# Kernel tuning notes

Hardware: AMD Instinct MI355X
Metric: run time of the kernel (lower is better)

## Reference

```python
import jax, jax.numpy as jnp
import numpy as np

# norse default LIFParameters / LIParameters constants
DT = 1e-3
TAU_SYN_INV = 200.0
TAU_MEM_INV = 100.0
V_LEAK = 0.0
V_TH = 1.0
V_RESET = 0.0
ALPHA = 100.0  # superspike surrogate-gradient slope


@jax.custom_vjp
def superspike(x):
    return (x > 0).astype(x.dtype)

def _ss_fwd(x):
    return (x > 0).astype(x.dtype), x

def _ss_bwd(x, g):
    return (g / (ALPHA * jnp.abs(x) + 1.0) ** 2,)

superspike.defvjp(_ss_fwd, _ss_bwd)


def lif_step(state, inp):
    """norse lif_feed_forward_step: decay v/i, spike on old current, then inject input."""
    v, i = state
    v_dec = v + DT * TAU_MEM_INV * ((V_LEAK - v) + i)
    i_dec = i - DT * TAU_SYN_INV * i
    z = superspike(v_dec - V_TH)
    v_new = (1.0 - z) * v_dec + z * V_RESET
    return z, (v_new, i_dec + inp)


def li_step(state, inp):
    """norse li_feed_forward_step: leaky integrator, output is the membrane voltage."""
    v, i = state
    v_new = v + DT * TAU_MEM_INV * ((V_LEAK - v) + i)
    i_new = i - DT * TAU_SYN_INV * i + inp
    return v_new, (v_new, i_new)


def setup_inputs() -> dict:
    key = jax.random.key(0)
    ks = jax.random.split(key, 5)
    B = 65536
    x = jax.random.normal(ks[0], (B, 1, 10, 10), dtype=jnp.float32)
    conv_w = jax.random.normal(ks[1], (2, 1, 4, 4), dtype=jnp.float32) * 0.3
    conv_b = jax.random.normal(ks[2], (2,), dtype=jnp.float32) * 0.1
    fc_w = jax.random.normal(ks[3], (10, 72), dtype=jnp.float32) * 0.1
    fc_b = jax.random.normal(ks[4], (10,), dtype=jnp.float32) * 0.1
    return {"x": x, "conv_w": conv_w, "conv_b": conv_b, "fc_w": fc_w, "fc_b": fc_b, "num_steps": 64}


def reference(x, conv_w, conv_b, fc_w, fc_b, num_steps):
    B = x.shape[0]
    out_dim = fc_w.shape[0]
    # static input: conv(x) identical at every step, hoist out of the time loop
    g = jax.lax.conv_general_dilated(
        x, conv_w, (1, 1), "VALID",
        dimension_numbers=("NCHW", "OIHW", "NCHW"),
    ) + conv_b[None, :, None, None]  # [B,2,7,7]

    def pool(z):  # MaxPool2d(kernel=2, stride=1), VALID
        return jax.lax.reduce_window(
            z, -jnp.inf, jax.lax.max, (1, 1, 2, 2), (1, 1, 1, 1), "VALID")

    s_lif0 = (jnp.zeros_like(g), jnp.zeros_like(g))                 # [B,2,7,7]
    s_li1_0 = (jnp.zeros((B, 2, 6, 6), x.dtype), jnp.zeros((B, 2, 6, 6), x.dtype))
    s_li2_0 = (jnp.zeros((B, out_dim), x.dtype), jnp.zeros((B, out_dim), x.dtype))

    def step(carry, _):
        s_lif, s1, s2 = carry
        z, s_lif = lif_step(s_lif, g)          # spikes [B,2,7,7]
        z = pool(z)                            # [B,2,6,6]
        z, s1 = li_step(s1, z)                 # LI voltage [B,2,6,6]
        z = z.reshape(B, -1)                   # [B,72]
        z = z @ fc_w.T + fc_b                  # [B,10]
        v, s2 = li_step(s2, z)                 # readout voltage [B,10]
        return (s_lif, s1, s2), None

    (s_lif, s1, s2), _ = jax.lax.scan(step, (s_lif0, s_li1_0, s_li2_0), None, length=num_steps)
    return s2[0]  # final readout membrane voltage [B, output_size]
```

## Files before the change

### kernel.cpp

```cpp
#include <hip/hip_runtime.h>

#define TMAX 64

__global__ __launch_bounds__(256) void snn_fused(
    const float* __restrict__ x,
    const float* __restrict__ conv_w,
    const float* __restrict__ conv_b,
    const float* __restrict__ fc_w,
    const float* __restrict__ fc_b,
    const int*   __restrict__ nsteps,
    float*       __restrict__ out,
    int B)
{
    __shared__ double d_F[TMAX];
    __shared__ float  s_r[TMAX];
    __shared__ float  s_rb[TMAX];
    __shared__ float  s_tab[8][256];
    __shared__ float  s_fcw[720];
    __shared__ float  s_fcb[16];
    __shared__ float  s_cb;

    const int tid = threadIdx.x;
    int T = nsteps[0];
    if (T > TMAX) T = TMAX;
    if (T < 0) T = 0;
    const int tlo = T < 32 ? T : 32;
    const int thi = T > 32 ? (T - 32) : 0;

    if (tid < TMAX) {
        double p9 = 1.0, p8 = 1.0;
        for (int k = 0; k < tid; ++k) { p9 *= 0.9; p8 *= 0.8; }
        d_F[tid] = p9 - p8;
    }
    for (int idx = tid; idx < 720; idx += 256) s_fcw[idx] = fc_w[idx];
    if (tid < 10) s_fcb[tid] = fc_b[tid];
    __syncthreads();

    if (tid < TMAX) {
        double r = 0.0;
        if (tid < T) {
            const int n = T - 1 - tid;
            for (int u = 0; u <= n; ++u) r += d_F[n - u] * d_F[u];
        }
        s_r[tid] = (float)r;
    }
    if (tid == 0) {
        double cb = 0.0;
        for (int m = 0; m < T; ++m) cb += d_F[m];
        s_cb = (float)cb;
    }
    __syncthreads();

    if (tid < 32) {
        s_rb[tid] = (tid < tlo) ? s_r[tlo - 1 - tid] : 0.f;
    } else if (tid < 64) {
        const int p = tid - 32;
        s_rb[tid] = (p < thi) ? s_r[tlo + thi - 1 - p] : 0.f;
    }
    __syncthreads();

    {
        const int v8 = tid;
        #pragma unroll
        for (int k = 0; k < 8; ++k) {
            float ssum = 0.f;
            #pragma unroll
            for (int bb = 0; bb < 8; ++bb)
                if ((v8 >> bb) & 1) ssum += s_rb[k * 8 + bb];
            s_tab[k][v8] = ssum;
        }
    }
    __syncthreads();

    const float cbsum = s_cb;

    const int gt  = blockIdx.x * 256 + tid;
    const int sub = gt & 15;
    const int b   = gt >> 4;
    const int c   = sub >> 3;
    const int y   = sub & 7;
    const int ysim = (y < 6) ? y : 6;
    if (b >= B) return;

    const float* xb = x + b * 100;
    const float cbias = conv_b[c];

    float gg7[7];
    #pragma unroll
    for (int xx = 0; xx < 7; ++xx) gg7[xx] = 0.f;
    {
        float wc[16];
        const float4* wq = reinterpret_cast<const float4*>(conv_w + c * 16);
        #pragma unroll
        for (int k = 0; k < 4; ++k) {
            float4 t = wq[k];
            wc[4*k+0] = t.x; wc[4*k+1] = t.y; wc[4*k+2] = t.z; wc[4*k+3] = t.w;
        }
        #pragma unroll
        for (int ky = 0; ky < 4; ++ky) {
            float xrow[10];
            const float2* q = reinterpret_cast<const float2*>(xb + (ysim + ky) * 10);
            #pragma unroll
            for (int k = 0; k < 5; ++k) { float2 t = q[k]; xrow[2*k] = t.x; xrow[2*k+1] = t.y; }
            #pragma unroll
            for (int xx = 0; xx < 7; ++xx) {
                float a = gg7[xx];
                #pragma unroll
                for (int kx = 0; kx < 4; ++kx)
                    a = __fadd_rn(a, __fmul_rn(wc[ky*4 + kx], xrow[xx + kx]));
                gg7[xx] = a;
            }
        }
    }
    #pragma unroll
    for (int xx = 0; xx < 7; ++xx) gg7[xx] = __fadd_rn(gg7[xx], cbias);

    float v[7], ii[7];
    unsigned int mlo[7], mhi[7];
    float fzero = 0.0f;
    #pragma unroll
    for (int xx = 0; xx < 7; ++xx) { v[xx] = 0.f; ii[xx] = 0.f; mlo[xx] = 0u; mhi[xx] = 0u; }

    #pragma unroll 4
    for (int t = 0; t < tlo; ++t) {
        #pragma unroll
        for (int xx = 0; xx < 7; ++xx) {
            const float imv  = __fsub_rn(ii[xx], v[xx]);
            const float vdec = __fadd_rn(v[xx], __fmul_rn(0.1f, imv));
            const float idec = __fsub_rn(ii[xx], __fmul_rn(0.2f, ii[xx]));
            float vnew;
            asm("v_cmp_lt_f32 vcc, 1.0, %[vd]\n\t"
                "v_cndmask_b32 %[vn], %[vd], %[vz], vcc\n\t"
                "v_addc_co_u32 %[mm], vcc, %[mm], %[mm], vcc"
                : [vn]"=v"(vnew), [mm]"+v"(mlo[xx])
                : [vd]"v"(vdec), [vz]"v"(fzero)
                : "vcc");
            v[xx]  = vnew;
            ii[xx] = __fadd_rn(idec, gg7[xx]);
        }
    }
    #pragma unroll 4
    for (int t = 0; t < thi; ++t) {
        #pragma unroll
        for (int xx = 0; xx < 7; ++xx) {
            const float imv  = __fsub_rn(ii[xx], v[xx]);
            const float vdec = __fadd_rn(v[xx], __fmul_rn(0.1f, imv));
            const float idec = __fsub_rn(ii[xx], __fmul_rn(0.2f, ii[xx]));
            float vnew;
            asm("v_cmp_lt_f32 vcc, 1.0, %[vd]\n\t"
                "v_cndmask_b32 %[vn], %[vd], %[vz], vcc\n\t"
                "v_addc_co_u32 %[mm], vcc, %[mm], %[mm], vcc"
                : [vn]"=v"(vnew), [mm]"+v"(mhi[xx])
                : [vd]"v"(vdec), [vz]"v"(fzero)
                : "vcc");
            v[xx]  = vnew;
            ii[xx] = __fadd_rn(idec, gg7[xx]);
        }
    }

    unsigned int nlo[7], nhi[7];
    #pragma unroll
    for (int xx = 0; xx < 7; ++xx) {
        nlo[xx] = __shfl_down(mlo[xx], 1);
        nhi[xx] = __shfl_down(mhi[xx], 1);
    }

    float outacc[10];
    #pragma unroll
    for (int o = 0; o < 10; ++o) outacc[o] = 0.f;

    if (y < 6) {
        const int jbase = c * 36 + y * 6;
        #pragma unroll
        for (int px = 0; px < 6; ++px) {
            const unsigned int pl = mlo[px] | mlo[px+1] | nlo[px] | nlo[px+1];
            const unsigned int ph = mhi[px] | mhi[px+1] | nhi[px] | nhi[px+1];
            float a = s_tab[0][pl & 255] + s_tab[1][(pl >> 8) & 255]
                    + s_tab[2][(pl >> 16) & 255] + s_tab[3][pl >> 24]
                    + s_tab[4][ph & 255] + s_tab[5][(ph >> 8) & 255]
                    + s_tab[6][(ph >> 16) & 255] + s_tab[7][ph >> 24];
            const int j = jbase + px;
            #pragma unroll
            for (int o = 0; o < 10; ++o)
                outacc[o] = fmaf(s_fcw[o * 72 + j], a, outacc[o]);
        }
    }

    #pragma unroll
    for (int o = 0; o < 10; ++o) {
        float t = outacc[o];
        t += __shfl_xor(t, 1);
        t += __shfl_xor(t, 2);
        t += __shfl_xor(t, 4);
        t += __shfl_xor(t, 8);
        if (sub == 0) out[b * 10 + o] = fmaf(cbsum, s_fcb[o], t);
    }
}

extern "C" void kernel_launch(void* const* d_in, const int* in_sizes, int n_in,
                              void* d_out, int out_size, void* d_ws, size_t ws_size,
                              hipStream_t stream) {
    const float* x      = (const float*)d_in[0];
    const float* conv_w = (const float*)d_in[1];
    const float* conv_b = (const float*)d_in[2];
    const float* fc_w   = (const float*)d_in[3];
    const float* fc_b   = (const float*)d_in[4];
    const int*   nsteps = (const int*)d_in[5];
    float* outp = (float*)d_out;

    const int B = in_sizes[0] / 100;
    const int total = 16 * B;
    const int block = 256;
    const int grid = (total + block - 1) / block;
    snn_fused<<<grid, block, 0, stream>>>(x, conv_w, conv_b, fc_w, fc_b, nsteps, outp, B);
}
```

Measured before the change: 83.30 us.

## Map 14 threads per sample and exchange spike masks via shared memory

Each sample now gets 14 threads (2 channels x 7 rows) instead of 16, so the two padding rows per sample no longer run the 64-step LIF simulation. Blocks grow to 896 threads covering 64 samples. The neighbour-row masks move through LDS instead of wave shuffles, and the per-sample readout reduction becomes an LDS write plus a serial 12-way sum instead of a butterfly shuffle. The extra __syncthreads calls, larger blocks and lower occupancy per CU may offset the cut in simulation work.

Measured after the change: 109.1 us. 30.9% more time.

```diff
diff --git a/kernel.cpp b/kernel.cpp
--- a/kernel.cpp
+++ b/kernel.cpp
@@ -1,8 +1,11 @@
 #include <hip/hip_runtime.h>
 
 #define TMAX 64
-
-__global__ __launch_bounds__(256) void snn_fused(
+#define BPB  64
+#define RPB  14
+#define NTHR (BPB * RPB)
+
+__global__ __launch_bounds__(NTHR) void snn_fused(
     const float* __restrict__ x,
     const float* __restrict__ conv_w,
     const float* __restrict__ conv_b,
@@ -19,6 +22,10 @@
     __shared__ float  s_fcw[720];
     __shared__ float  s_fcb[16];
     __shared__ float  s_cb;
+    __shared__ union {
+        uint2 masks[BPB * RPB * 7];
+        float red[BPB * 12 * 10];
+    } u;
 
     const int tid = threadIdx.x;
     int T = nsteps[0];
@@ -32,7 +39,7 @@
         for (int k = 0; k < tid; ++k) { p9 *= 0.9; p8 *= 0.8; }
         d_F[tid] = p9 - p8;
     }
-    for (int idx = tid; idx < 720; idx += 256) s_fcw[idx] = fc_w[idx];
+    for (int idx = tid; idx < 720; idx += NTHR) s_fcw[idx] = fc_w[idx];
     if (tid < 10) s_fcb[tid] = fc_b[tid];
     __syncthreads();
 
@@ -40,7 +47,7 @@
         double r = 0.0;
         if (tid < T) {
             const int n = T - 1 - tid;
-            for (int u = 0; u <= n; ++u) r += d_F[n - u] * d_F[u];
+            for (int uu = 0; uu <= n; ++uu) r += d_F[n - uu] * d_F[uu];
         }
         s_r[tid] = (float)r;
     }
@@ -59,7 +66,7 @@
     }
     __syncthreads();
 
-    {
+    if (tid < 256) {
         const int v8 = tid;
         #pragma unroll
         for (int k = 0; k < 8; ++k) {
@@ -74,15 +81,14 @@
 
     const float cbsum = s_cb;
 
-    const int gt  = blockIdx.x * 256 + tid;
-    const int sub = gt & 15;
-    const int b   = gt >> 4;
-    const int c   = sub >> 3;
-    const int y   = sub & 7;
-    const int ysim = (y < 6) ? y : 6;
-    if (b >= B) return;
-
-    const float* xb = x + b * 100;
+    const int bl = tid / RPB;
+    const int r  = tid - bl * RPB;
+    const int c  = r / 7;
+    const int y  = r - c * 7;
+    const int b  = blockIdx.x * BPB + bl;
+    const int bc = (b < B) ? b : (B - 1);
+
+    const float* xb = x + bc * 100;
     const float cbias = conv_b[c];
 
     float gg7[7];
@@ -99,7 +105,7 @@
         #pragma unroll
         for (int ky = 0; ky < 4; ++ky) {
             float xrow[10];
-            const float2* q = reinterpret_cast<const float2*>(xb + (ysim + ky) * 10);
+            const float2* q = reinterpret_cast<const float2*>(xb + (y + ky) * 10);
             #pragma unroll
             for (int k = 0; k < 5; ++k) { float2 t = q[k]; xrow[2*k] = t.x; xrow[2*k+1] = t.y; }
             #pragma unroll
@@ -158,23 +164,28 @@
         }
     }
 
-    unsigned int nlo[7], nhi[7];
-    #pragma unroll
-    for (int xx = 0; xx < 7; ++xx) {
-        nlo[xx] = __shfl_down(mlo[xx], 1);
-        nhi[xx] = __shfl_down(mhi[xx], 1);
-    }
+    {
+        uint2* mrow = &u.masks[(bl * RPB + r) * 7];
+        #pragma unroll
+        for (int xx = 0; xx < 7; ++xx) mrow[xx] = make_uint2(mlo[xx], mhi[xx]);
+    }
+    __syncthreads();
 
     float outacc[10];
     #pragma unroll
     for (int o = 0; o < 10; ++o) outacc[o] = 0.f;
 
     if (y < 6) {
+        const uint2* nrow = &u.masks[(bl * RPB + c * 7 + y + 1) * 7];
+        uint2 nb[7];
+        #pragma unroll
+        for (int xx = 0; xx < 7; ++xx) nb[xx] = nrow[xx];
+
         const int jbase = c * 36 + y * 6;
         #pragma unroll
         for (int px = 0; px < 6; ++px) {
-            const unsigned int pl = mlo[px] | mlo[px+1] | nlo[px] | nlo[px+1];
-            const unsigned int ph = mhi[px] | mhi[px+1] | nhi[px] | nhi[px+1];
+            const unsigned int pl = mlo[px] | mlo[px+1] | nb[px].x | nb[px+1].x;
+            const unsigned int ph = mhi[px] | mhi[px+1] | nb[px].y | nb[px+1].y;
             float a = s_tab[0][pl & 255] + s_tab[1][(pl >> 8) & 255]
                     + s_tab[2][(pl >> 16) & 255] + s_tab[3][pl >> 24]
                     + s_tab[4][ph & 255] + s_tab[5][(ph >> 8) & 255]
@@ -185,15 +196,26 @@
                 outacc[o] = fmaf(s_fcw[o * 72 + j], a, outacc[o]);
         }
     }
-
-    #pragma unroll
-    for (int o = 0; o < 10; ++o) {
-        float t = outacc[o];
-        t += __shfl_xor(t, 1);
-        t += __shfl_xor(t, 2);
-        t += __shfl_xor(t, 4);
-        t += __shfl_xor(t, 8);
-        if (sub == 0) out[b * 10 + o] = fmaf(cbsum, s_fcb[o], t);
+    __syncthreads();
+
+    if (y < 6) {
+        float* dst = &u.red[(bl * 12 + c * 6 + y) * 10];
+        #pragma unroll
+        for (int o = 0; o < 10; ++o) dst[o] = outacc[o];
+    }
+    __syncthreads();
+
+    if (tid < BPB * 10) {
+        const int bl2 = tid / 10;
+        const int o   = tid - bl2 * 10;
+        const int b2  = blockIdx.x * BPB + bl2;
+        if (b2 < B) {
+            float s = 0.f;
+            #pragma unroll
+            for (int pr = 0; pr < 12; ++pr)
+                s += u.red[(bl2 * 12 + pr) * 10 + o];
+            out[b2 * 10 + o] = fmaf(cbsum, s_fcb[o], s);
+        }
     }
 }
 
@@ -209,8 +231,6 @@
     float* outp = (float*)d_out;
 
     const int B = in_sizes[0] / 100;
-    const int total = 16 * B;
-    const int block = 256;
-    const int grid = (total + block - 1) / block;
-    snn_fused<<<grid, block, 0, stream>>>(x, conv_w, conv_b, fc_w, fc_b, nsteps, outp, B);
+    const int grid = (B + BPB - 1) / BPB;
+    snn_fused<<<grid, NTHR, 0, stream>>>(x, conv_w, conv_b, fc_w, fc_b, nsteps, outp, B);
 }
```
